# Kernel tuning notes

Measured on AMD Instinct MI355X. Metric: run time of the kernel, lower is better.

## Reference

```python
import jax, jax.numpy as jnp
import numpy as np

EPS = 1e-12      # LayerNorm eps in Selector
TAU = 1e-6       # gumbel-softmax temperature
TOPK = 2         # seg_selector.topk
TOPJ = 128       # reg_selector.topk
NUMC, NUMF_PER_C, NUMP, DIM, QDIM = 4, 4, 256, 1024, 512


def _ln(x, g, b):
    m = x.mean(-1, keepdims=True)
    v = ((x - m) ** 2).mean(-1, keepdims=True)
    return (x - m) / jnp.sqrt(v + EPS) * g + b


def _selector(q, K, V_flat, Wq, bq, ln_q_g, ln_q_b, Wk, bk, ln_k_g, ln_k_b, topk, key):
    # q: (B, qdim); K: (B, n, dim); V_flat: (B, n, F)
    Qp = _ln(q @ Wq.T + bq, ln_q_g, ln_q_b)                      # (B, dim)
    Kp = _ln(K @ Wk.T + bk, ln_k_g, ln_k_b)                      # (B, n, dim)
    probs = jax.nn.softmax(jnp.einsum('bnd,bd->bn', Kp, Qp), axis=-1)  # (B, n)
    B, n = probs.shape
    # F.gumbel_softmax applied to the softmax probs (as in the torch code),
    # vectorized over the topk loop: one mask per selection round.
    u = jax.random.uniform(key, (B, topk, n), minval=1e-20, maxval=1.0)
    g = -jnp.log(-jnp.log(u))
    masks = jax.nn.softmax((probs[:, None, :] + g) / TAU, axis=-1)     # (B, topk, n)
    return jnp.einsum('btn,bnf->btf', masks, V_flat)                   # (B, topk, F)


def setup_inputs() -> dict:
    key = jax.random.key(0)
    ks = jax.random.split(key, 24)
    bz = 8
    s = 0.02
    d = {
        'q_feat': jax.random.normal(ks[0], (bz, QDIM, 1), dtype=jnp.float32),
        'image_embeds': jax.random.normal(ks[1], (bz, NUMC, NUMF_PER_C, NUMP, DIM), dtype=jnp.float32),
        'video_cls': jax.random.normal(ks[2], (bz, NUMC * NUMF_PER_C, DIM), dtype=jnp.float32),
        # seg_selector params
        'seg_Wq': s * jax.random.normal(ks[3], (DIM, QDIM), dtype=jnp.float32),
        'seg_bq': jnp.zeros((DIM,), jnp.float32),
        'seg_ln_q_g': jnp.ones((DIM,), jnp.float32),
        'seg_ln_q_b': jnp.zeros((DIM,), jnp.float32),
        'seg_Wk': s * jax.random.normal(ks[4], (DIM, DIM), dtype=jnp.float32),
        'seg_bk': jnp.zeros((DIM,), jnp.float32),
        'seg_ln_k_g': jnp.ones((DIM,), jnp.float32),
        'seg_ln_k_b': jnp.zeros((DIM,), jnp.float32),
        # reg_selector params
        'reg_Wq': s * jax.random.normal(ks[5], (DIM, QDIM), dtype=jnp.float32),
        'reg_bq': jnp.zeros((DIM,), jnp.float32),
        'reg_ln_q_g': jnp.ones((DIM,), jnp.float32),
        'reg_ln_q_b': jnp.zeros((DIM,), jnp.float32),
        'reg_Wk': s * jax.random.normal(ks[6], (DIM, DIM), dtype=jnp.float32),
        'reg_bk': jnp.zeros((DIM,), jnp.float32),
        'reg_ln_k_g': jnp.ones((DIM,), jnp.float32),
        'reg_ln_k_b': jnp.zeros((DIM,), jnp.float32),
    }
    return d


def reference(q_feat, image_embeds, video_cls,
              seg_Wq, seg_bq, seg_ln_q_g, seg_ln_q_b, seg_Wk, seg_bk, seg_ln_k_g, seg_ln_k_b,
              reg_Wq, reg_bq, reg_ln_q_g, reg_ln_q_b, reg_Wk, reg_bk, reg_ln_k_g, reg_ln_k_b):
    bz = q_feat.shape[0]
    # video_in.view(bz, numc*numf, nump, -1); hdim == dim so no projections
    video_feat = image_embeds.reshape(bz, NUMC * NUMF_PER_C, NUMP, DIM)
    vc = video_cls / jnp.linalg.norm(video_cls, axis=-1, keepdims=True)
    seg_feat = vc.reshape(bz, NUMC, NUMF_PER_C, DIM).mean(axis=2)        # (bz, numc, dim)
    # CLIP text feature, L2-normalized (get_clip_txt_embedding)
    q = q_feat[..., 0]
    q = q / jnp.linalg.norm(q, axis=-1, keepdims=True)                   # (bz, qdim)

    k1, k2 = jax.random.split(jax.random.key(42))
    # seg_selector: K=seg_feat (bz,4,dim), V=video_feat viewed (bz,4, 4*256*1024)
    sel = _selector(q, seg_feat, video_feat.reshape(bz, NUMC, -1),
                    seg_Wq, seg_bq, seg_ln_q_g, seg_ln_q_b,
                    seg_Wk, seg_bk, seg_ln_k_g, seg_ln_k_b, TOPK, k1)
    sel = sel.reshape(bz, TOPK * NUMF_PER_C, NUMP, DIM)                  # (bz, 8, 256, 1024)

    # reg_selector over the flattened pseudo-batch (bz*8)
    B2 = bz * TOPK * NUMF_PER_C
    K2 = sel.reshape(B2, NUMP, DIM)
    q2 = jnp.repeat(q, TOPK * NUMF_PER_C, axis=0)                        # (bz*8, qdim)
    sel2 = _selector(q2, K2, K2, reg_Wq, reg_bq, reg_ln_q_g, reg_ln_q_b,
                     reg_Wk, reg_bk, reg_ln_k_g, reg_ln_k_b, TOPJ, k2)   # (bz*8, 128, 1024)

    return sel2.reshape(bz, 1, TOPK * NUMF_PER_C, TOPJ, DIM)
```

## Files before the change

### kernel.cpp

```cpp
#include <hip/hip_runtime.h>
#include <hip/hip_fp16.h>
#include <stdint.h>

#ifndef JAX_PARTITIONABLE
#define JAX_PARTITIONABLE 1
#endif

typedef _Float16 f16x8 __attribute__((ext_vector_type(8)));
typedef float    f32x4 __attribute__((ext_vector_type(4)));

static constexpr int BZ   = 8;
static constexpr int QD   = 512;
static constexpr int DIM  = 1024;
static constexpr int I2   = 64;
static constexpr int TOPJ = 128;
static constexpr int NROW = 16384;
static constexpr int NCT  = 4;

static constexpr size_t EAI = 0;
static constexpr size_t EWI = (size_t)33554432;
static constexpr size_t FQN   = 17825792;
static constexpr size_t FSF   = FQN + 4096;
static constexpr size_t FYS   = FSF + 32768;
static constexpr size_t FYR   = FYS + 8192;
static constexpr size_t FY2   = FYR + 8192;
static constexpr size_t FGQ   = FY2 + 32768;
static constexpr size_t FSG   = FGQ + 8192;
static constexpr size_t FCL   = FSG + 8;
static constexpr size_t FMS   = FCL + 8;
static constexpr size_t FP2   = FMS + 64;
static constexpr size_t FPART = FP2 + 16384;

__device__ __forceinline__ uint32_t rotl32(uint32_t v, int d){ return (v << d) | (v >> (32 - d)); }

__device__ __forceinline__ void tf2x32(uint32_t k0, uint32_t k1, uint32_t x0, uint32_t x1,
                                       uint32_t& o0, uint32_t& o1){
  const uint32_t ks2 = k0 ^ k1 ^ 0x1BD11BDAu;
  x0 += k0; x1 += k1;
#define TFR(r) x0 += x1; x1 = rotl32(x1, r); x1 ^= x0;
  TFR(13) TFR(15) TFR(26) TFR(6)
  x0 += k1;  x1 += ks2 + 1u;
  TFR(17) TFR(29) TFR(16) TFR(24)
  x0 += ks2; x1 += k0 + 2u;
  TFR(13) TFR(15) TFR(26) TFR(6)
  x0 += k0;  x1 += k1 + 3u;
  TFR(17) TFR(29) TFR(16) TFR(24)
  x0 += k1;  x1 += ks2 + 4u;
  TFR(13) TFR(15) TFR(26) TFR(6)
  x0 += ks2; x1 += k0 + 5u;
#undef TFR
  o0 = x0; o1 = x1;
}

__device__ __forceinline__ void jax_keys(uint32_t& k1a, uint32_t& k1b, uint32_t& k2a, uint32_t& k2b){
#if JAX_PARTITIONABLE
  uint32_t a,b,c,d;
  tf2x32(0u, 42u, 0u, 0u, a, b);
  tf2x32(0u, 42u, 0u, 1u, c, d);
  k1a = a; k1b = b; k2a = c; k2b = d;
#else
  uint32_t a,b,c,d;
  tf2x32(0u, 42u, 0u, 2u, a, b);
  tf2x32(0u, 42u, 1u, 3u, c, d);
  k1a = a; k1b = c; k2a = b; k2b = d;
#endif
}

__device__ __forceinline__ float jax_uniform(uint32_t ka, uint32_t kb, uint32_t idx, uint32_t half_n){
  uint32_t o0, o1, bits;
#if JAX_PARTITIONABLE
  (void)half_n;
  tf2x32(ka, kb, 0u, idx, o0, o1);
  bits = o0 ^ o1;
#else
  if (idx < half_n){ tf2x32(ka, kb, idx, idx + half_n, o0, o1); bits = o0; }
  else             { tf2x32(ka, kb, idx - half_n, idx, o0, o1); bits = o1; }
#endif
  float f = __uint_as_float((bits >> 9) | 0x3f800000u) - 1.0f;
  f = f + 1e-20f;
  return fmaxf(f, 1e-20f);
}

__device__ __forceinline__ float blk_sum(float v, float* red){
  const int tid = threadIdx.x;
  red[tid] = v; __syncthreads();
  #pragma unroll
  for (int s = 128; s > 0; s >>= 1){
    if (tid < s) red[tid] += red[tid + s];
    __syncthreads();
  }
  float r = red[0]; __syncthreads();
  return r;
}
__device__ __forceinline__ float blk_max(float v, float* red){
  const int tid = threadIdx.x;
  red[tid] = v; __syncthreads();
  #pragma unroll
  for (int s = 128; s > 0; s >>= 1){
    if (tid < s) red[tid] = fmaxf(red[tid], red[tid + s]);
    __syncthreads();
  }
  float r = red[0]; __syncthreads();
  return r;
}

__device__ __forceinline__ unsigned short f2h(float x){
  return __half_as_ushort(__float2half(x));
}
__device__ __forceinline__ float h2f(unsigned short u){
  return __half2float(__ushort_as_half(u));
}

__device__ __forceinline__ void gl_lds16(const void* g, void* l){
  __builtin_amdgcn_global_load_lds((const __attribute__((address_space(1))) void*)g,
                                   (__attribute__((address_space(3))) void*)l, 16, 0, 0);
}

__global__ __launch_bounds__(256) void k_norm(const float* __restrict__ qf,
                                              const float* __restrict__ vcls,
                                              float* __restrict__ ws)
{
  const int b = blockIdx.x, tid = threadIdx.x;
  __shared__ float red[256];
  float q0 = qf[b * QD + tid];
  float q1 = qf[b * QD + 256 + tid];
  float ss = blk_sum(q0*q0 + q1*q1, red);
  float nrm = sqrtf(ss);
  ws[FQN + (size_t)b * QD + tid]       = q0 / nrm;
  ws[FQN + (size_t)b * QD + 256 + tid] = q1 / nrm;

  float sf[4][4];
  #pragma unroll
  for (int c = 0; c < 4; ++c)
    #pragma unroll
    for (int r = 0; r < 4; ++r) sf[c][r] = 0.f;

  for (int f = 0; f < 16; ++f){
    float v[4]; float s2 = 0.f;
    #pragma unroll
    for (int r = 0; r < 4; ++r){
      v[r] = vcls[((size_t)(b * 16 + f)) * DIM + tid + (r << 8)];
      s2 += v[r] * v[r];
    }
    float s = blk_sum(s2, red);
    float n2 = sqrtf(s);
    const int c = f >> 2;
    #pragma unroll
    for (int r = 0; r < 4; ++r) sf[c][r] += v[r] / n2;
  }
  #pragma unroll
  for (int c = 0; c < 4; ++c)
    #pragma unroll
    for (int r = 0; r < 4; ++r)
      ws[FSF + ((size_t)(b * 4 + c)) * DIM + tid + (r << 8)] = sf[c][r] * 0.25f;
}

__global__ __launch_bounds__(256) void k_matvec(
    const float* __restrict__ sWq, const float* __restrict__ sbq,
    const float* __restrict__ rWq, const float* __restrict__ rbq,
    const float* __restrict__ sWk, const float* __restrict__ sbk,
    float* __restrict__ ws)
{
  const int bid = blockIdx.x;
  const int b = bid >> 5, ch = bid & 31;
  const int tid = threadIdx.x;
  const int di = tid >> 3, sub = tid & 7;
  const int d = ch * 32 + di;
  const float* qn = ws + FQN + (size_t)b * QD;
  const float* sf = ws + FSF + (size_t)b * 4 * DIM;

  {
    const float* wr = sWq + (size_t)d * QD + sub * 64;
    const float* qq = qn + sub * 64;
    float a = 0.f;
    #pragma unroll
    for (int e = 0; e < 64; e += 4){
      float4 w4 = *(const float4*)(wr + e);
      a += qq[e]*w4.x + qq[e+1]*w4.y + qq[e+2]*w4.z + qq[e+3]*w4.w;
    }
    a += __shfl_xor(a, 1); a += __shfl_xor(a, 2); a += __shfl_xor(a, 4);
    if (sub == 0) ws[FYS + (size_t)b * DIM + d] = a + sbq[d];
  }
  {
    const float* wr = rWq + (size_t)d * QD + sub * 64;
    const float* qq = qn + sub * 64;
    float a = 0.f;
    #pragma unroll
    for (int e = 0; e < 64; e += 4){
      float4 w4 = *(const float4*)(wr + e);
      a += qq[e]*w4.x + qq[e+1]*w4.y + qq[e+2]*w4.z + qq[e+3]*w4.w;
    }
    a += __shfl_xor(a, 1); a += __shfl_xor(a, 2); a += __shfl_xor(a, 4);
    if (sub == 0) ws[FYR + (size_t)b * DIM + d] = a + rbq[d];
  }
  for (int c = 0; c < 4; ++c){
    const float* wr = sWk + (size_t)d * DIM + sub * 128;
    const float* qq = sf + (size_t)c * DIM + sub * 128;
    float a = 0.f;
    #pragma unroll
    for (int e = 0; e < 128; e += 4){
      float4 w4 = *(const float4*)(wr + e);
      a += qq[e]*w4.x + qq[e+1]*w4.y + qq[e+2]*w4.z + qq[e+3]*w4.w;
    }
    a += __shfl_xor(a, 1); a += __shfl_xor(a, 2); a += __shfl_xor(a, 4);
    if (sub == 0) ws[FY2 + ((size_t)(b * 4 + c)) * DIM + d] = a + sbk[d];
  }
}

__global__ __launch_bounds__(256) void k_post(
    const float* __restrict__ slnqg, const float* __restrict__ slnqb,
    const float* __restrict__ rlnqg, const float* __restrict__ rlnqb,
    const float* __restrict__ rlnkg, const float* __restrict__ rlnkb,
    const float* __restrict__ slnkg, const float* __restrict__ slnkb,
    float* __restrict__ ws)
{
  const int b = blockIdx.x, tid = threadIdx.x;
  __shared__ float red[256];
  __shared__ float qps[DIM];
  __shared__ float lg[4];

  {
    float y[4];
    #pragma unroll
    for (int r = 0; r < 4; ++r) y[r] = ws[FYS + (size_t)b * DIM + tid + (r << 8)];
    float S = blk_sum(y[0]+y[1]+y[2]+y[3], red);
    float mu = S * (1.f / 1024.f);
    float pv = 0.f;
    #pragma unroll
    for (int r = 0; r < 4; ++r){ float dv = y[r]-mu; pv += dv*dv; }
    float V = blk_sum(pv, red);
    float sig = sqrtf(V * (1.f / 1024.f) + 1e-12f);
    #pragma unroll
    for (int r = 0; r < 4; ++r){
      const int d = tid + (r << 8);
      qps[d] = (y[r]-mu)/sig * slnqg[d] + slnqb[d];
    }
  }
  __syncthreads();

  {
    float y[4];
    #pragma unroll
    for (int r = 0; r < 4; ++r) y[r] = ws[FYR + (size_t)b * DIM + tid + (r << 8)];
    float S = blk_sum(y[0]+y[1]+y[2]+y[3], red);
    float mu = S * (1.f / 1024.f);
    float pv = 0.f;
    #pragma unroll
    for (int r = 0; r < 4; ++r){ float dv = y[r]-mu; pv += dv*dv; }
    float V = blk_sum(pv, red);
    float sig = sqrtf(V * (1.f / 1024.f) + 1e-12f);
    float sg = 0.f, cl = 0.f;
    #pragma unroll
    for (int r = 0; r < 4; ++r){
      const int d = tid + (r << 8);
      float o = (y[r]-mu)/sig * rlnqg[d] + rlnqb[d];
      float gv = rlnkg[d] * o;
      ws[FGQ + (size_t)b * DIM + d] = gv;
      sg += gv;
      cl += rlnkb[d] * o;
    }
    float SG = blk_sum(sg, red);
    float CL = blk_sum(cl, red);
    if (tid == 0){ ws[FSG + b] = SG; ws[FCL + b] = CL; }
  }

  for (int c = 0; c < 4; ++c){
    float y[4];
    #pragma unroll
    for (int r = 0; r < 4; ++r) y[r] = ws[FY2 + ((size_t)(b * 4 + c)) * DIM + tid + (r << 8)];
    float S = blk_sum(y[0]+y[1]+y[2]+y[3], red);
    float mu = S * (1.f / 1024.f);
    float pv = 0.f;
    #pragma unroll
    for (int r = 0; r < 4; ++r){ float dv = y[r]-mu; pv += dv*dv; }
    float V = blk_sum(pv, red);
    float sig = sqrtf(V * (1.f / 1024.f) + 1e-12f);
    float lp = 0.f;
    #pragma unroll
    for (int r = 0; r < 4; ++r){
      const int d = tid + (r << 8);
      float kp = (y[r]-mu)/sig * slnkg[d] + slnkb[d];
      lp += kp * qps[d];
    }
    float L = blk_sum(lp, red);
    if (tid == 0) lg[c] = L;
  }
  __syncthreads();

  if (tid == 0){
    float m = fmaxf(fmaxf(lg[0], lg[1]), fmaxf(lg[2], lg[3]));
    float e[4], s = 0.f;
    #pragma unroll
    for (int c = 0; c < 4; ++c){ e[c] = expf(lg[c] - m); s += e[c]; }
    float probs[4];
    #pragma unroll
    for (int c = 0; c < 4; ++c) probs[c] = e[c] / s;
    uint32_t k1a, k1b, k2a, k2b;
    jax_keys(k1a, k1b, k2a, k2b);
    for (int t = 0; t < 2; ++t){
      float x[4];
      #pragma unroll
      for (int c = 0; c < 4; ++c){
        float u = jax_uniform(k1a, k1b, (uint32_t)(b * 8 + t * 4 + c), 32u);
        float gmb = -logf(-logf(u));
        x[c] = (probs[c] + gmb) / 1e-6f;
      }
      float xm = fmaxf(fmaxf(x[0], x[1]), fmaxf(x[2], x[3]));
      float w[4], sw = 0.f;
      #pragma unroll
      for (int c = 0; c < 4; ++c){ w[c] = expf(x[c] - xm); sw += w[c]; }
      #pragma unroll
      for (int c = 0; c < 4; ++c) ws[FMS + b * 8 + t * 4 + c] = w[c] / sw;
    }
  }
}

__global__ __launch_bounds__(256) void k_sel(const float* __restrict__ E,
                                             const float* __restrict__ W,
                                             float* __restrict__ ws)
{
  const int bid = blockIdx.x;
  const int th = threadIdx.x;
  const int kc = th >> 3;
  const int c  = (th & 7) >> 1;
  const int pos = (th & 1) * 4;

  if (bid < I2 * 256){
    const int i = bid >> 8, p = bid & 255;
    const int bz = i >> 3, it = i & 7, t = it >> 2, j = it & 3;
    const int row = i * 256 + p;
    const int d = th << 2;
    const float* msk = ws + FMS + bz * 8 + t * 4;
    float4 a = {0.f, 0.f, 0.f, 0.f};
    #pragma unroll
    for (int cc = 0; cc < 4; ++cc){
      const float w = msk[cc];
      if (w != 0.f){
        const float4 v = *(const float4*)&E[(((size_t)((bz * 4 + cc) * 4 + j)) * 256 + p) * DIM + d];
        a.x += w * v.x; a.y += w * v.y; a.z += w * v.z; a.w += w * v.w;
      }
    }
    unsigned short* AI = (unsigned short*)ws + EAI;
    ushort4 h, l;
    h.x = f2h(a.x); l.x = f2h(a.x - h2f(h.x));
    h.y = f2h(a.y); l.y = f2h(a.y - h2f(h.y));
    h.z = f2h(a.z); l.z = f2h(a.z - h2f(h.z));
    h.w = f2h(a.w); l.w = f2h(a.w - h2f(h.w));
    const size_t base = ((size_t)kc * NROW + row) * 64;
    *(ushort4*)&AI[base + c * 8 + pos]      = h;
    *(ushort4*)&AI[base + c * 8 + pos + 32] = l;
  } else {
    const int row = bid - I2 * 256;
    unsigned short* WI = (unsigned short*)ws + EWI;
    float4 v = *(const float4*)&W[(size_t)row * DIM + th * 4];
    ushort4 h, l;
    h.x = f2h(v.x); l.x = f2h(v.x - h2f(h.x));
    h.y = f2h(v.y); l.y = f2h(v.y - h2f(h.y));
    h.z = f2h(v.z); l.z = f2h(v.z - h2f(h.z));
    h.w = f2h(v.w); l.w = f2h(v.w - h2f(h.w));
    const size_t base = ((size_t)kc * 1024 + row) * 64;
    *(ushort4*)&WI[base + c * 8 + pos]      = h;
    *(ushort4*)&WI[base + c * 8 + pos + 32] = l;
  }
}

__global__ __launch_bounds__(512, 2) void k_gemm(const float* __restrict__ bk,
                                                 float* __restrict__ ws)
{
  const unsigned short* AI = (const unsigned short*)ws + EAI;
  const unsigned short* WI = (const unsigned short*)ws + EWI;
  const float* gq = ws + FGQ;
  float* part = ws + FPART;

  __shared__ __align__(16) unsigned short Abuf[2][16384];
  __shared__ __align__(16) unsigned short Bbuf[2][16384];

  const int bid = blockIdx.x;
  const int xcd = bid & 7, g = bid >> 3;
  const int rt = xcd * 8 + (g >> 2);
  const int ct = g & 3;
  const int R0 = rt * 256, C0 = ct * 256;
  const int tid = threadIdx.x;
  const int lane = tid & 63, wid = tid >> 6;
  const int wr = wid >> 2, wc = wid & 3;
  const int b = R0 >> 11;

  const int src_off = (lane >> 3) * 64 + (((lane & 7) ^ (lane >> 3)) << 3);
  const int pcH = ((lane >> 4) ^ (lane & 7)) * 16;
  const int pcL = pcH ^ 64;
  const int raw = wr * 128 + (lane & 15);
  const int rbw = wc * 64 + (lane & 15);

  f32x4 acc[8][4];
  #pragma unroll
  for (int m = 0; m < 8; ++m)
    #pragma unroll
    for (int n = 0; n < 4; ++n)
      acc[m][n] = (f32x4){0.f, 0.f, 0.f, 0.f};

  auto stage = [&](int buf, int kc){
    const unsigned short* As = AI + ((size_t)kc * NROW + R0 + wid * 32) * 64 + src_off;
    const unsigned short* Bs = WI + ((size_t)kc * 1024 + C0 + wid * 32) * 64 + src_off;
    unsigned short* Ad = &Abuf[buf][wid * 2048];
    unsigned short* Bd = &Bbuf[buf][wid * 2048];
    #pragma unroll
    for (int q = 0; q < 4; ++q) gl_lds16(As + q * 512, Ad + q * 512);
    #pragma unroll
    for (int q = 0; q < 4; ++q) gl_lds16(Bs + q * 512, Bd + q * 512);
  };

  stage(0, 0);
  asm volatile("s_waitcnt vmcnt(0)" ::: "memory");
  __builtin_amdgcn_s_barrier();

  f16x8 bh[4], bl[4], ah0[4], al0[4], ah1[4], al1[4];

  #pragma unroll 1
  for (int kc = 0; kc < 32; ++kc){
    const int cur = kc & 1;
    const char* pa = (const char*)&Abuf[cur][0];
    const char* pb = (const char*)&Bbuf[cur][0];
    if (kc < 31) stage(cur ^ 1, kc + 1);

    #pragma unroll
    for (int f = 0; f < 4; ++f){
      const int ro = (rbw + f * 16) << 7;
      bh[f] = *(const f16x8*)(pb + ro + pcH);
      bl[f] = *(const f16x8*)(pb + ro + pcL);
    }
    #pragma unroll
    for (int f = 0; f < 4; ++f){
      const int ro = (raw + f * 16) << 7;
      ah0[f] = *(const f16x8*)(pa + ro + pcH);
      al0[f] = *(const f16x8*)(pa + ro + pcL);
    }
    asm volatile("s_waitcnt lgkmcnt(0)" ::: "memory");
    __builtin_amdgcn_sched_barrier(0);
    __builtin_amdgcn_s_setprio(1);
    #pragma unroll
    for (int m = 0; m < 4; ++m)
      #pragma unroll
      for (int n = 0; n < 4; ++n){
        acc[m][n] = __builtin_amdgcn_mfma_f32_16x16x32_f16(ah0[m], bh[n], acc[m][n], 0, 0, 0);
        acc[m][n] = __builtin_amdgcn_mfma_f32_16x16x32_f16(ah0[m], bl[n], acc[m][n], 0, 0, 0);
        acc[m][n] = __builtin_amdgcn_mfma_f32_16x16x32_f16(al0[m], bh[n], acc[m][n], 0, 0, 0);
      }
    __builtin_amdgcn_s_setprio(0);

    #pragma unroll
    for (int f = 0; f < 4; ++f){
      const int ro = (raw + 64 + f * 16) << 7;
      ah1[f] = *(const f16x8*)(pa + ro + pcH);
      al1[f] = *(const f16x8*)(pa + ro + pcL);
    }
    asm volatile("s_waitcnt lgkmcnt(0)" ::: "memory");
    __builtin_amdgcn_sched_barrier(0);
    __builtin_amdgcn_s_setprio(1);
    #pragma unroll
    for (int m = 0; m < 4; ++m)
      #pragma unroll
      for (int n = 0; n < 4; ++n){
        acc[m + 4][n] = __builtin_amdgcn_mfma_f32_16x16x32_f16(ah1[m], bh[n], acc[m + 4][n], 0, 0, 0);
        acc[m + 4][n] = __builtin_amdgcn_mfma_f32_16x16x32_f16(ah1[m], bl[n], acc[m + 4][n], 0, 0, 0);
        acc[m + 4][n] = __builtin_amdgcn_mfma_f32_16x16x32_f16(al1[m], bh[n], acc[m + 4][n], 0, 0, 0);
      }
    __builtin_amdgcn_s_setprio(0);

    asm volatile("s_waitcnt vmcnt(0)" ::: "memory");
    __builtin_amdgcn_sched_barrier(0);
    __builtin_amdgcn_s_barrier();
  }

  float bkv[4], gv[4];
  #pragma unroll
  for (int n = 0; n < 4; ++n){
    const int col = C0 + wc * 64 + n * 16 + (lane & 15);
    bkv[n] = bk[col];
    gv[n]  = gq[(size_t)b * DIM + col];
  }
  float* fred = (float*)&Abuf[0][0];
  #pragma unroll
  for (int m = 0; m < 8; ++m)
    #pragma unroll
    for (int r = 0; r < 4; ++r){
      float s = 0.f, q = 0.f, tv = 0.f;
      #pragma unroll
      for (int n = 0; n < 4; ++n){
        float y = acc[m][n][r] + bkv[n];
        s += y; q += y * y; tv += y * gv[n];
      }
      #pragma unroll
      for (int msk = 8; msk >= 1; msk >>= 1){
        s += __shfl_xor(s, msk); q += __shfl_xor(q, msk); tv += __shfl_xor(tv, msk);
      }
      if ((lane & 15) == 0){
        const int rl = wr * 128 + m * 16 + (lane >> 4) * 4 + r;
        fred[(rl * 4 + wc) * 3 + 0] = s;
        fred[(rl * 4 + wc) * 3 + 1] = q;
        fred[(rl * 4 + wc) * 3 + 2] = tv;
      }
    }
  __syncthreads();
  if (tid < 256){
    #pragma unroll
    for (int st = 0; st < 3; ++st){
      float v = fred[(tid * 4 + 0) * 3 + st] + fred[(tid * 4 + 1) * 3 + st]
              + fred[(tid * 4 + 2) * 3 + st] + fred[(tid * 4 + 3) * 3 + st];
      part[((size_t)ct * NROW + R0 + tid) * 3 + st] = v;
    }
  }
}

__global__ __launch_bounds__(256) void k_probs2(float* __restrict__ ws)
{
  const int i = blockIdx.x, tid = threadIdx.x;
  const int r = i * 256 + tid;
  const int b = i >> 3;
  __shared__ float red[256];
  const float* part = ws + FPART;
  float S = 0.f, Q = 0.f, T = 0.f;
  #pragma unroll
  for (int ct = 0; ct < NCT; ++ct){
    const float* pp = part + ((size_t)ct * NROW + r) * 3;
    S += pp[0]; Q += pp[1]; T += pp[2];
  }
  float mu  = S * (1.f / 1024.f);
  float var = Q * (1.f / 1024.f) - mu * mu;
  float sig = sqrtf(var + 1e-12f);
  float L = (T - mu * ws[FSG + b]) / sig + ws[FCL + b];
  float M = blk_max(L, red);
  float w = expf(L - M);
  float sw = blk_sum(w, red);
  ws[FP2 + r] = w / sw;
}

__global__ __launch_bounds__(256) void k_out(const float* __restrict__ E,
                                             const float* __restrict__ ws,
                                             float* __restrict__ out)
{
  const int bid = blockIdx.x;
  const int i = bid >> 7, t2 = bid & 127;
  const int bz = i >> 3, it = i & 7, tt = it >> 2, j = it & 3;
  const int tid = threadIdx.x;
  __shared__ float red[256];
  __shared__ float wv[256];
  __shared__ float mloc[4];
  __shared__ unsigned long long mk[4];

  if (tid < 4) mloc[tid] = ws[FMS + bz * 8 + tt * 4 + tid];

  uint32_t k1a, k1b, k2a, k2b;
  jax_keys(k1a, k1b, k2a, k2b);
  const uint32_t fidx = ((uint32_t)(i * TOPJ + t2)) * 256u + (uint32_t)tid;
  float u = jax_uniform(k2a, k2b, fidx, 1048576u);
  float gmb = -logf(-logf(u));
  float x = (ws[FP2 + (size_t)i * 256 + tid] + gmb) / 1e-6f;
  float M = blk_max(x, red);
  float w = expf(x - M);
  float sw = blk_sum(w, red);
  float wn = w / sw;
  wv[tid] = wn;
  unsigned long long bal = __ballot(wn != 0.f);
  if ((tid & 63) == 0) mk[tid >> 6] = bal;
  __syncthreads();

  const int d = tid << 2;
  float4 acc = {0.f, 0.f, 0.f, 0.f};
  for (int wq = 0; wq < 4; ++wq){
    unsigned long long mm = mk[wq];
    while (mm){
      const int l = __ffsll(mm) - 1;
      mm &= mm - 1;
      const int p = (wq << 6) + l;
      const float wp = wv[p];
      #pragma unroll
      for (int c = 0; c < 4; ++c){
        const float mc = mloc[c];
        if (mc != 0.f){
          const float4 v = *(const float4*)&E[(((size_t)((bz * 4 + c) * 4 + j)) * 256 + p) * DIM + d];
          const float wm = wp * mc;
          acc.x += wm * v.x; acc.y += wm * v.y; acc.z += wm * v.z; acc.w += wm * v.w;
        }
      }
    }
  }
  *(float4*)&out[((size_t)(i * TOPJ + t2)) * DIM + d] = acc;
}

extern "C" void kernel_launch(void* const* d_in, const int* in_sizes, int n_in,
                              void* d_out, int out_size, void* d_ws, size_t ws_size,
                              hipStream_t stream)
{
  const float* qf    = (const float*)d_in[0];
  const float* E     = (const float*)d_in[1];
  const float* vcls  = (const float*)d_in[2];
  const float* sWq   = (const float*)d_in[3];
  const float* sbq   = (const float*)d_in[4];
  const float* slnqg = (const float*)d_in[5];
  const float* slnqb = (const float*)d_in[6];
  const float* sWk   = (const float*)d_in[7];
  const float* sbk   = (const float*)d_in[8];
  const float* slnkg = (const float*)d_in[9];
  const float* slnkb = (const float*)d_in[10];
  const float* rWq   = (const float*)d_in[11];
  const float* rbq   = (const float*)d_in[12];
  const float* rlnqg = (const float*)d_in[13];
  const float* rlnqb = (const float*)d_in[14];
  const float* rWk   = (const float*)d_in[15];
  const float* rbk   = (const float*)d_in[16];
  const float* rlnkg = (const float*)d_in[17];
  const float* rlnkb = (const float*)d_in[18];
  float* ws  = (float*)d_ws;
  float* out = (float*)d_out;

  k_norm<<<BZ, 256, 0, stream>>>(qf, vcls, ws);
  k_matvec<<<256, 256, 0, stream>>>(sWq, sbq, rWq, rbq, sWk, sbk, ws);
  k_post<<<BZ, 256, 0, stream>>>(slnqg, slnqb, rlnqg, rlnqb, rlnkg, rlnkb, slnkg, slnkb, ws);
  k_sel<<<I2 * 256 + 1024, 256, 0, stream>>>(E, rWk, ws);
  k_gemm<<<256, 512, 0, stream>>>(rbk, ws);
  k_probs2<<<I2, 256, 0, stream>>>(ws);
  k_out<<<I2 * TOPJ, 256, 0, stream>>>(E, ws, out);
}
```

Before: 197.6 us.

## Use 4-wave 128x128 warp tiles in k_gemm with double-buffered B fragments

Rebuilds the split-fp16 GEMM block from 8 waves to 4 waves. Each wave now computes a 128x128 sub-tile (8x8 MFMA accumulators) instead of 128x64, which cuts LDS reads per MFMA: all 8 A fragments are loaded once and the B fragments are ping-ponged, with the next column's fragment prefetched during the current MFMA group. Staging per wave doubles to cover the same 256x256 block tile, and the cross-wave reduction now sums 2 column partials instead of 4. The cost is much higher register pressure (256 accumulator floats plus fragments) and fewer waves per CU to hide latency.

Measured after the change: 201.5 us. No clear change (+2.0%).

```diff
diff --git a/kernel.cpp b/kernel.cpp
--- a/kernel.cpp
+++ b/kernel.cpp
@@ -364,7 +364,7 @@
   }
 }
 
-__global__ __launch_bounds__(512, 2) void k_gemm(const float* __restrict__ bk,
+__global__ __launch_bounds__(256, 1) void k_gemm(const float* __restrict__ bk,
                                                  float* __restrict__ ws)
 {
   const unsigned short* AI = (const unsigned short*)ws + EAI;
@@ -382,38 +382,39 @@
   const int R0 = rt * 256, C0 = ct * 256;
   const int tid = threadIdx.x;
   const int lane = tid & 63, wid = tid >> 6;
-  const int wr = wid >> 2, wc = wid & 3;
+  const int wr = wid >> 1, wc = wid & 1;
   const int b = R0 >> 11;
 
   const int src_off = (lane >> 3) * 64 + (((lane & 7) ^ (lane >> 3)) << 3);
   const int pcH = ((lane >> 4) ^ (lane & 7)) * 16;
   const int pcL = pcH ^ 64;
   const int raw = wr * 128 + (lane & 15);
-  const int rbw = wc * 64 + (lane & 15);
-
-  f32x4 acc[8][4];
+  const int rbw = wc * 128 + (lane & 15);
+
+  f32x4 acc[8][8];
   #pragma unroll
   for (int m = 0; m < 8; ++m)
     #pragma unroll
-    for (int n = 0; n < 4; ++n)
+    for (int n = 0; n < 8; ++n)
       acc[m][n] = (f32x4){0.f, 0.f, 0.f, 0.f};
 
   auto stage = [&](int buf, int kc){
-    const unsigned short* As = AI + ((size_t)kc * NROW + R0 + wid * 32) * 64 + src_off;
-    const unsigned short* Bs = WI + ((size_t)kc * 1024 + C0 + wid * 32) * 64 + src_off;
-    unsigned short* Ad = &Abuf[buf][wid * 2048];
-    unsigned short* Bd = &Bbuf[buf][wid * 2048];
-    #pragma unroll
-    for (int q = 0; q < 4; ++q) gl_lds16(As + q * 512, Ad + q * 512);
-    #pragma unroll
-    for (int q = 0; q < 4; ++q) gl_lds16(Bs + q * 512, Bd + q * 512);
+    const unsigned short* As = AI + ((size_t)kc * NROW + R0 + wid * 64) * 64 + src_off;
+    const unsigned short* Bs = WI + ((size_t)kc * 1024 + C0 + wid * 64) * 64 + src_off;
+    unsigned short* Ad = &Abuf[buf][wid * 4096];
+    unsigned short* Bd = &Bbuf[buf][wid * 4096];
+    #pragma unroll
+    for (int q = 0; q < 8; ++q) gl_lds16(As + q * 512, Ad + q * 512);
+    #pragma unroll
+    for (int q = 0; q < 8; ++q) gl_lds16(Bs + q * 512, Bd + q * 512);
   };
 
   stage(0, 0);
   asm volatile("s_waitcnt vmcnt(0)" ::: "memory");
   __builtin_amdgcn_s_barrier();
 
-  f16x8 bh[4], bl[4], ah0[4], al0[4], ah1[4], al1[4];
+  f16x8 Ah[8], Al[8];
+  f16x8 bh[2], bl[2];
 
   #pragma unroll 1
   for (int kc = 0; kc < 32; ++kc){
@@ -423,58 +424,48 @@
     if (kc < 31) stage(cur ^ 1, kc + 1);
 
     #pragma unroll
-    for (int f = 0; f < 4; ++f){
-      const int ro = (rbw + f * 16) << 7;
-      bh[f] = *(const f16x8*)(pb + ro + pcH);
-      bl[f] = *(const f16x8*)(pb + ro + pcL);
-    }
-    #pragma unroll
-    for (int f = 0; f < 4; ++f){
+    for (int f = 0; f < 8; ++f){
       const int ro = (raw + f * 16) << 7;
-      ah0[f] = *(const f16x8*)(pa + ro + pcH);
-      al0[f] = *(const f16x8*)(pa + ro + pcL);
+      Ah[f] = *(const f16x8*)(pa + ro + pcH);
+      Al[f] = *(const f16x8*)(pa + ro + pcL);
+    }
+    {
+      const int ro = rbw << 7;
+      bh[0] = *(const f16x8*)(pb + ro + pcH);
+      bl[0] = *(const f16x8*)(pb + ro + pcL);
     }
     asm volatile("s_waitcnt lgkmcnt(0)" ::: "memory");
     __builtin_amdgcn_sched_barrier(0);
-    __builtin_amdgcn_s_setprio(1);
-    #pragma unroll
-    for (int m = 0; m < 4; ++m)
+
+    #pragma unroll
+    for (int fn = 0; fn < 8; ++fn){
+      const int pcur = fn & 1, pnxt = pcur ^ 1;
+      if (fn < 7){
+        const int ro = (rbw + (fn + 1) * 16) << 7;
+        bh[pnxt] = *(const f16x8*)(pb + ro + pcH);
+        bl[pnxt] = *(const f16x8*)(pb + ro + pcL);
+      }
+      __builtin_amdgcn_s_setprio(1);
       #pragma unroll
-      for (int n = 0; n < 4; ++n){
-        acc[m][n] = __builtin_amdgcn_mfma_f32_16x16x32_f16(ah0[m], bh[n], acc[m][n], 0, 0, 0);
-        acc[m][n] = __builtin_amdgcn_mfma_f32_16x16x32_f16(ah0[m], bl[n], acc[m][n], 0, 0, 0);
-        acc[m][n] = __builtin_amdgcn_mfma_f32_16x16x32_f16(al0[m], bh[n], acc[m][n], 0, 0, 0);
-      }
-    __builtin_amdgcn_s_setprio(0);
-
-    #pragma unroll
-    for (int f = 0; f < 4; ++f){
-      const int ro = (raw + 64 + f * 16) << 7;
-      ah1[f] = *(const f16x8*)(pa + ro + pcH);
-      al1[f] = *(const f16x8*)(pa + ro + pcL);
-    }
-    asm volatile("s_waitcnt lgkmcnt(0)" ::: "memory");
-    __builtin_amdgcn_sched_barrier(0);
-    __builtin_amdgcn_s_setprio(1);
-    #pragma unroll
-    for (int m = 0; m < 4; ++m)
-      #pragma unroll
-      for (int n = 0; n < 4; ++n){
-        acc[m + 4][n] = __builtin_amdgcn_mfma_f32_16x16x32_f16(ah1[m], bh[n], acc[m + 4][n], 0, 0, 0);
-        acc[m + 4][n] = __builtin_amdgcn_mfma_f32_16x16x32_f16(ah1[m], bl[n], acc[m + 4][n], 0, 0, 0);
-        acc[m + 4][n] = __builtin_amdgcn_mfma_f32_16x16x32_f16(al1[m], bh[n], acc[m + 4][n], 0, 0, 0);
-      }
-    __builtin_amdgcn_s_setprio(0);
+      for (int m = 0; m < 8; ++m){
+        acc[m][fn] = __builtin_amdgcn_mfma_f32_16x16x32_f16(Ah[m], bh[pcur], acc[m][fn], 0, 0, 0);
+        acc[m][fn] = __builtin_amdgcn_mfma_f32_16x16x32_f16(Ah[m], bl[pcur], acc[m][fn], 0, 0, 0);
+        acc[m][fn] = __builtin_amdgcn_mfma_f32_16x16x32_f16(Al[m], bh[pcur], acc[m][fn], 0, 0, 0);
+      }
+      __builtin_amdgcn_s_setprio(0);
+      asm volatile("s_waitcnt lgkmcnt(0)" ::: "memory");
+      __builtin_amdgcn_sched_barrier(0);
+    }
 
     asm volatile("s_waitcnt vmcnt(0)" ::: "memory");
     __builtin_amdgcn_sched_barrier(0);
     __builtin_amdgcn_s_barrier();
   }
 
-  float bkv[4], gv[4];
-  #pragma unroll
-  for (int n = 0; n < 4; ++n){
-    const int col = C0 + wc * 64 + n * 16 + (lane & 15);
+  float bkv[8], gv[8];
+  #pragma unroll
+  for (int n = 0; n < 8; ++n){
+    const int col = C0 + wc * 128 + n * 16 + (lane & 15);
     bkv[n] = bk[col];
     gv[n]  = gq[(size_t)b * DIM + col];
   }
@@ -485,7 +476,7 @@
     for (int r = 0; r < 4; ++r){
       float s = 0.f, q = 0.f, tv = 0.f;
       #pragma unroll
-      for (int n = 0; n < 4; ++n){
+      for (int n = 0; n < 8; ++n){
         float y = acc[m][n][r] + bkv[n];
         s += y; q += y * y; tv += y * gv[n];
       }
@@ -495,17 +486,16 @@
       }
       if ((lane & 15) == 0){
         const int rl = wr * 128 + m * 16 + (lane >> 4) * 4 + r;
-        fred[(rl * 4 + wc) * 3 + 0] = s;
-        fred[(rl * 4 + wc) * 3 + 1] = q;
-        fred[(rl * 4 + wc) * 3 + 2] = tv;
+        fred[(rl * 2 + wc) * 3 + 0] = s;
+        fred[(rl * 2 + wc) * 3 + 1] = q;
+        fred[(rl * 2 + wc) * 3 + 2] = tv;
       }
     }
   __syncthreads();
   if (tid < 256){
     #pragma unroll
     for (int st = 0; st < 3; ++st){
-      float v = fred[(tid * 4 + 0) * 3 + st] + fred[(tid * 4 + 1) * 3 + st]
-              + fred[(tid * 4 + 2) * 3 + st] + fred[(tid * 4 + 3) * 3 + st];
+      float v = fred[(tid * 2 + 0) * 3 + st] + fred[(tid * 2 + 1) * 3 + st];
       part[((size_t)ct * NROW + R0 + tid) * 3 + st] = v;
     }
   }
@@ -617,7 +607,7 @@
   k_matvec<<<256, 256, 0, stream>>>(sWq, sbq, rWq, rbq, sWk, sbk, ws);
   k_post<<<BZ, 256, 0, stream>>>(slnqg, slnqb, rlnqg, rlnqb, rlnkg, rlnkb, slnkg, slnkb, ws);
   k_sel<<<I2 * 256 + 1024, 256, 0, stream>>>(E, rWk, ws);
-  k_gemm<<<256, 512, 0, stream>>>(rbk, ws);
+  k_gemm<<<256, 256, 0, stream>>>(rbk, ws);
   k_probs2<<<I2, 256, 0, stream>>>(ws);
   k_out<<<I2 * TOPJ, 256, 0, stream>>>(E, ws, out);
 }
```

## Split GEMM main loop into four barrier-separated quadrants with staggered A/B prefetch

Applied to the files above, without the earlier changes.

Restructures the k_gemm inner loop into four MFMA phases (2x2 quadrants of the wave tile), reusing a single set of A/B fragment registers and splitting the next-tile global-to-LDS prefetch into separate A and B stages interleaved between phases. It also removes the occupancy-2 launch bound, freeing the compiler to use more registers per thread. The intent is to cut register pressure from fragment buffers and spread memory issue across the loop to overlap better with MFMA work. It adds several extra workgroup barriers per iteration, which could serialize waves, and may drop occupancy to one block per CU.

Measured after the change: 192.4 us. -2.6%, faster.

```diff
diff --git a/kernel.cpp b/kernel.cpp
--- a/kernel.cpp
+++ b/kernel.cpp
@@ -364,8 +364,8 @@
   }
 }
 
-__global__ __launch_bounds__(512, 2) void k_gemm(const float* __restrict__ bk,
-                                                 float* __restrict__ ws)
+__global__ __launch_bounds__(512) void k_gemm(const float* __restrict__ bk,
+                                              float* __restrict__ ws)
 {
   const unsigned short* AI = (const unsigned short*)ws + EAI;
   const unsigned short* WI = (const unsigned short*)ws + EWI;
@@ -398,74 +398,113 @@
     for (int n = 0; n < 4; ++n)
       acc[m][n] = (f32x4){0.f, 0.f, 0.f, 0.f};
 
-  auto stage = [&](int buf, int kc){
+  auto stageA = [&](int buf, int kc){
     const unsigned short* As = AI + ((size_t)kc * NROW + R0 + wid * 32) * 64 + src_off;
+    unsigned short* Ad = &Abuf[buf][wid * 2048];
+    #pragma unroll
+    for (int q = 0; q < 4; ++q) gl_lds16(As + q * 512, Ad + q * 512);
+  };
+  auto stageB = [&](int buf, int kc){
     const unsigned short* Bs = WI + ((size_t)kc * 1024 + C0 + wid * 32) * 64 + src_off;
-    unsigned short* Ad = &Abuf[buf][wid * 2048];
     unsigned short* Bd = &Bbuf[buf][wid * 2048];
-    #pragma unroll
-    for (int q = 0; q < 4; ++q) gl_lds16(As + q * 512, Ad + q * 512);
     #pragma unroll
     for (int q = 0; q < 4; ++q) gl_lds16(Bs + q * 512, Bd + q * 512);
   };
 
-  stage(0, 0);
+  stageA(0, 0);
+  stageB(0, 0);
   asm volatile("s_waitcnt vmcnt(0)" ::: "memory");
   __builtin_amdgcn_s_barrier();
 
-  f16x8 bh[4], bl[4], ah0[4], al0[4], ah1[4], al1[4];
+  f16x8 ah[4], al[4], bh[4], bl[4];
 
   #pragma unroll 1
   for (int kc = 0; kc < 32; ++kc){
     const int cur = kc & 1;
     const char* pa = (const char*)&Abuf[cur][0];
     const char* pb = (const char*)&Bbuf[cur][0];
-    if (kc < 31) stage(cur ^ 1, kc + 1);
 
     #pragma unroll
     for (int f = 0; f < 4; ++f){
+      const int ro = (raw + f * 16) << 7;
+      ah[f] = *(const f16x8*)(pa + ro + pcH);
+      al[f] = *(const f16x8*)(pa + ro + pcL);
+    }
+    #pragma unroll
+    for (int f = 0; f < 2; ++f){
       const int ro = (rbw + f * 16) << 7;
       bh[f] = *(const f16x8*)(pb + ro + pcH);
       bl[f] = *(const f16x8*)(pb + ro + pcL);
     }
-    #pragma unroll
-    for (int f = 0; f < 4; ++f){
-      const int ro = (raw + f * 16) << 7;
-      ah0[f] = *(const f16x8*)(pa + ro + pcH);
-      al0[f] = *(const f16x8*)(pa + ro + pcL);
-    }
+    if (kc < 31) stageA(cur ^ 1, kc + 1);
+    __builtin_amdgcn_s_barrier();
     asm volatile("s_waitcnt lgkmcnt(0)" ::: "memory");
     __builtin_amdgcn_sched_barrier(0);
     __builtin_amdgcn_s_setprio(1);
     #pragma unroll
     for (int m = 0; m < 4; ++m)
       #pragma unroll
-      for (int n = 0; n < 4; ++n){
-        acc[m][n] = __builtin_amdgcn_mfma_f32_16x16x32_f16(ah0[m], bh[n], acc[m][n], 0, 0, 0);
-        acc[m][n] = __builtin_amdgcn_mfma_f32_16x16x32_f16(ah0[m], bl[n], acc[m][n], 0, 0, 0);
-        acc[m][n] = __builtin_amdgcn_mfma_f32_16x16x32_f16(al0[m], bh[n], acc[m][n], 0, 0, 0);
+      for (int n = 0; n < 2; ++n){
+        acc[m][n] = __builtin_amdgcn_mfma_f32_16x16x32_f16(ah[m], bh[n], acc[m][n], 0, 0, 0);
+        acc[m][n] = __builtin_amdgcn_mfma_f32_16x16x32_f16(ah[m], bl[n], acc[m][n], 0, 0, 0);
+        acc[m][n] = __builtin_amdgcn_mfma_f32_16x16x32_f16(al[m], bh[n], acc[m][n], 0, 0, 0);
       }
     __builtin_amdgcn_s_setprio(0);
-
-    #pragma unroll
-    for (int f = 0; f < 4; ++f){
-      const int ro = (raw + 64 + f * 16) << 7;
-      ah1[f] = *(const f16x8*)(pa + ro + pcH);
-      al1[f] = *(const f16x8*)(pa + ro + pcL);
-    }
+    __builtin_amdgcn_s_barrier();
+
+    #pragma unroll
+    for (int f = 2; f < 4; ++f){
+      const int ro = (rbw + f * 16) << 7;
+      bh[f] = *(const f16x8*)(pb + ro + pcH);
+      bl[f] = *(const f16x8*)(pb + ro + pcL);
+    }
+    if (kc < 31) stageB(cur ^ 1, kc + 1);
+    __builtin_amdgcn_s_barrier();
     asm volatile("s_waitcnt lgkmcnt(0)" ::: "memory");
     __builtin_amdgcn_sched_barrier(0);
     __builtin_amdgcn_s_setprio(1);
     #pragma unroll
     for (int m = 0; m < 4; ++m)
       #pragma unroll
-      for (int n = 0; n < 4; ++n){
-        acc[m + 4][n] = __builtin_amdgcn_mfma_f32_16x16x32_f16(ah1[m], bh[n], acc[m + 4][n], 0, 0, 0);
-        acc[m + 4][n] = __builtin_amdgcn_mfma_f32_16x16x32_f16(ah1[m], bl[n], acc[m + 4][n], 0, 0, 0);
-        acc[m + 4][n] = __builtin_amdgcn_mfma_f32_16x16x32_f16(al1[m], bh[n], acc[m + 4][n], 0, 0, 0);
+      for (int n = 2; n < 4; ++n){
+        acc[m][n] = __builtin_amdgcn_mfma_f32_16x16x32_f16(ah[m], bh[n], acc[m][n], 0, 0, 0);
+        acc[m][n] = __builtin_amdgcn_mfma_f32_16x16x32_f16(ah[m], bl[n], acc[m][n], 0, 0, 0);
+        acc[m][n] = __builtin_amdgcn_mfma_f32_16x16x32_f16(al[m], bh[n], acc[m][n], 0, 0, 0);
       }
     __builtin_amdgcn_s_setprio(0);
-
+    __builtin_amdgcn_s_barrier();
+
+    #pragma unroll
+    for (int f = 0; f < 4; ++f){
+      const int ro = (raw + 64 + f * 16) << 7;
+      ah[f] = *(const f16x8*)(pa + ro + pcH);
+      al[f] = *(const f16x8*)(pa + ro + pcL);
+    }
+    __builtin_amdgcn_s_barrier();
+    asm volatile("s_waitcnt lgkmcnt(0)" ::: "memory");
+    __builtin_amdgcn_sched_barrier(0);
+    __builtin_amdgcn_s_setprio(1);
+    #pragma unroll
+    for (int m = 0; m < 4; ++m)
+      #pragma unroll
+      for (int n = 0; n < 2; ++n){
+        acc[m + 4][n] = __builtin_amdgcn_mfma_f32_16x16x32_f16(ah[m], bh[n], acc[m + 4][n], 0, 0, 0);
+        acc[m + 4][n] = __builtin_amdgcn_mfma_f32_16x16x32_f16(ah[m], bl[n], acc[m + 4][n], 0, 0, 0);
+        acc[m + 4][n] = __builtin_amdgcn_mfma_f32_16x16x32_f16(al[m], bh[n], acc[m + 4][n], 0, 0, 0);
+      }
+    __builtin_amdgcn_s_setprio(0);
+    __builtin_amdgcn_s_barrier();
+
+    __builtin_amdgcn_s_setprio(1);
+    #pragma unroll
+    for (int m = 0; m < 4; ++m)
+      #pragma unroll
+      for (int n = 2; n < 4; ++n){
+        acc[m + 4][n] = __builtin_amdgcn_mfma_f32_16x16x32_f16(ah[m], bh[n], acc[m + 4][n], 0, 0, 0);
+        acc[m + 4][n] = __builtin_amdgcn_mfma_f32_16x16x32_f16(ah[m], bl[n], acc[m + 4][n], 0, 0, 0);
+        acc[m + 4][n] = __builtin_amdgcn_mfma_f32_16x16x32_f16(al[m], bh[n], acc[m + 4][n], 0, 0, 0);
+      }
+    __builtin_amdgcn_s_setprio(0);
     asm volatile("s_waitcnt vmcnt(0)" ::: "memory");
     __builtin_amdgcn_sched_barrier(0);
     __builtin_amdgcn_s_barrier();
```
